# Kernel tuning notes

Hardware: AMD Instinct MI355X
Metric: run time of the kernel (lower is better)

Reference implementation:

```python
import jax, jax.numpy as jnp
import numpy as np

N_NODES = 50000
K_MAX = 10
BATCH = 64
T = 32
N_INPUTS = 16
BITS_PER_FEATURE = 4
INPUT_BITS = N_INPUTS * BITS_PER_FEATURE  # 64


def setup_inputs() -> dict:
    key = jax.random.key(0)
    ks = jax.random.split(key, 8)
    x = jax.random.randint(ks[0], (BATCH, T, INPUT_BITS), 0, 2, dtype=jnp.int32)
    adj_list = jax.random.randint(ks[1], (N_NODES, K_MAX), 0, N_NODES, dtype=jnp.int32)
    adj_list_mask = jax.random.randint(ks[2], (N_NODES, K_MAX), 0, 2, dtype=jnp.int32)
    lut = jax.random.randint(ks[3], (N_NODES, 2 ** K_MAX), 0, 2, dtype=jnp.int32)
    init_states = jax.random.randint(ks[4], (N_NODES,), 0, 2, dtype=jnp.int32)
    input_nodes = jax.random.randint(ks[5], (INPUT_BITS,), 0, N_NODES, dtype=jnp.int32)
    W = jax.random.normal(ks[6], (N_INPUTS, N_NODES), dtype=jnp.float32) * (1.0 / np.sqrt(N_NODES))
    b = jax.random.normal(ks[7], (N_INPUTS,), dtype=jnp.float32) * 0.01
    return {"x": x, "adj_list": adj_list, "adj_list_mask": adj_list_mask,
            "lut": lut, "init_states": init_states, "input_nodes": input_nodes,
            "W": W, "b": b}


def reference(x, adj_list, adj_list_mask, lut, init_states, input_nodes, W, b):
    B, T_, _ = x.shape
    N, K = adj_list.shape
    # powers_of_2 = 2**arange(K).flip()  (MSB-first bit packing)
    pow2 = (2 ** jnp.arange(K - 1, -1, -1)).astype(jnp.int32)  # [K]
    node_ids = jnp.arange(N, dtype=jnp.int32)  # [N]
    s0 = jnp.broadcast_to(init_states[None, :], (B, N)).astype(jnp.int32)

    def step(states, x_t):
        # xor input perturbation at input_nodes
        cur = states[:, input_nodes]                      # [B, INPUT_BITS]
        states = states.at[:, input_nodes].set(jnp.bitwise_xor(cur, x_t))
        # gather masked neighbor states and bit-pack into LUT index
        neigh = jnp.take(states, adj_list, axis=1)        # [B, N, K]
        idx = jnp.sum(neigh * adj_list_mask[None] * pow2, axis=-1)  # [B, N]
        new_states = lut[node_ids[None, :], idx]          # [B, N]
        return new_states, None

    final_states, _ = jax.lax.scan(step, s0, jnp.moveaxis(x, 1, 0))
    # readout = nn.Linear(n_nodes, n_inputs) on final binary states
    out = final_states.astype(jnp.float32) @ W.T + b      # [B, N_INPUTS]
    return out
```

## Files before the change

kernel.cpp:

```cpp
#include <hip/hip_runtime.h>
#include <stdint.h>

#define N_NODES    50000
#define K_MAX      10
#define BATCH      64
#define T_STEPS    32
#define N_INPUTS   16
#define INPUT_BITS 64

#define NPW   256
#define NWG   196
#define NTHR  1024
#define NBUF  (T_STEPS + 1)

#define BUF_STRIDE_B 400128u

#define OFF_BUFS   0u
#define OFF_XMASK  (NBUF * BUF_STRIDE_B)
#define OFF_CTR    (OFF_XMASK + 16384u)
#define OFF_PLUT   (OFF_CTR + 128u)

__global__ void prep_kernel(const int* __restrict__ x,
                            const int* __restrict__ init_states,
                            const int* __restrict__ input_nodes,
                            uint64_t* __restrict__ bufs,
                            uint64_t* __restrict__ xmask,
                            uint32_t* __restrict__ ctr) {
    const int gid = blockIdx.x * blockDim.x + threadIdx.x;
    const size_t strw = BUF_STRIDE_B / 8;
    if (gid < N_NODES) {
        int n = gid;
        int jm = -1;
        for (int j = 0; j < INPUT_BITS; ++j)
            if (input_nodes[j] == n) jm = j;
        uint64_t v = init_states[n] ? ~0ull : 0ull;
        if (jm >= 0) {
            uint64_t m = 0ull;
            for (int b = 0; b < BATCH; ++b)
                m |= (uint64_t)(x[b * (T_STEPS * INPUT_BITS) + jm] & 1) << b;
            v ^= m;
        }
        bufs[n] = v;
    } else if (gid < N_NODES + NBUF) {
        bufs[(size_t)(gid - N_NODES) * strw + N_NODES] = 0ull;
    } else if (gid < N_NODES + NBUF + T_STEPS * INPUT_BITS) {
        int k = gid - (N_NODES + NBUF);
        int t = k >> 6, j = k & 63;
        uint64_t m = 0ull;
        for (int b = 0; b < BATCH; ++b)
            m |= (uint64_t)(x[b * (T_STEPS * INPUT_BITS) + t * INPUT_BITS + j] & 1) << b;
        xmask[k] = m;
    } else if (gid < N_NODES + NBUF + T_STEPS * INPUT_BITS + T_STEPS) {
        ctr[gid - (N_NODES + NBUF + T_STEPS * INPUT_BITS)] = 0;
    }
}

__global__ void lutpack_kernel(const int* __restrict__ lut,
                               uint64_t* __restrict__ plut) {
    const int tid = threadIdx.x;
    const int blk = blockIdx.x;
    const int lane = tid & 63, wave = tid >> 6;
    int v = lut[(size_t)blk * 1024 + tid];
    uint64_t m = __ballot(v & 1);
    if (lane == 0) plut[(size_t)blk * 16 + wave] = m;
}

__global__ __launch_bounds__(NTHR)
void reservoir_coop(const uint64_t* __restrict__ plut,
                    const int* __restrict__ adj,
                    const int* __restrict__ adjmask,
                    const int* __restrict__ input_nodes,
                    const uint64_t* __restrict__ xmask,
                    uint64_t* __restrict__ bufs,
                    uint32_t* __restrict__ ctr) {
    __shared__ uint8_t lutb[NPW * 128];

    const int tid = threadIdx.x;
    const int wg  = blockIdx.x;

    {
        const uint4* src = (const uint4*)(plut + (size_t)wg * NPW * 16);
        uint4* dst = (uint4*)lutb;
        dst[tid * 2]     = src[tid * 2];
        dst[tid * 2 + 1] = src[tid * 2 + 1];
    }

    const int nl   = tid >> 2;
    const int q    = tid & 3;
    const int node = wg * NPW + nl;
    const bool valid = node < N_NODES;
    const uint32_t qsh = (uint32_t)(q & 1) * 16;

    uint32_t off[K_MAX];
    uint32_t soff = 0;
    int jm = -1;
    if (valid) {
        #pragma unroll
        for (int k = 0; k < K_MAX; ++k) {
            int a  = adj[node * K_MAX + k];
            int mk = adjmask[node * K_MAX + k];
            off[k] = (uint32_t)(mk ? a : N_NODES) * 8u + (uint32_t)(q >> 1) * 4u;
        }
        for (int j = 0; j < INPUT_BITS; ++j)
            if (input_nodes[j] == node) jm = j;
        soff = (uint32_t)node * 8u + (uint32_t)(q >> 1) * 4u;
    }
    const int rowbase = nl * 128;
    __syncthreads();

    for (int t = 0; t < T_STEPS; ++t) {
        const char* src = (const char*)bufs + (size_t)t * BUF_STRIDE_B;
        char*       dst = (char*)bufs + (size_t)(t + 1) * BUF_STRIDE_B;
        if (valid) {
            uint32_t w[K_MAX];
            #pragma unroll
            for (int k = 0; k < K_MAX; ++k)
                w[k] = *(const uint32_t*)(src + off[k]) >> qsh;

            uint32_t o16 = 0;
            #pragma unroll
            for (int b = 0; b < 16; ++b) {
                uint32_t idx = 0;
                #pragma unroll
                for (int k = 0; k < K_MAX; ++k)
                    idx = (idx << 1) | ((w[k] >> b) & 1u);
                uint32_t d = *(const uint32_t*)(lutb + rowbase + ((idx >> 5) << 2));
                o16 |= ((d >> (idx & 31)) & 1u) << b;
            }

            uint32_t hi = __shfl_down(o16, 1);
            if ((q & 1) == 0) {
                uint32_t o32 = o16 | (hi << 16);
                if (jm >= 0 && t < T_STEPS - 1)
                    o32 ^= ((const uint32_t*)xmask)[((t + 1) * INPUT_BITS + jm) * 2 + (q >> 1)];
                __hip_atomic_store((uint32_t*)(dst + soff), o32,
                                   __ATOMIC_RELAXED, __HIP_MEMORY_SCOPE_AGENT);
            }
        }

        if (t < T_STEPS - 1) {
            __syncthreads();
            if (tid == 0) {
                __hip_atomic_fetch_add(&ctr[t], 1u, __ATOMIC_RELAXED, __HIP_MEMORY_SCOPE_AGENT);
                while (__hip_atomic_load(&ctr[t], __ATOMIC_RELAXED, __HIP_MEMORY_SCOPE_AGENT)
                       < (uint32_t)NWG)
                    __builtin_amdgcn_s_sleep(2);
            }
            __syncthreads();
        }
    }
}

__global__ void out_kernel(const uint64_t* __restrict__ fstate,
                           const float* __restrict__ W,
                           const float* __restrict__ bias,
                           float* __restrict__ out) {
    const int wg = blockIdx.x;
    const int b = wg >> 4, i = wg & 15;
    const int tid = threadIdx.x;
    const uint8_t* st = (const uint8_t*)fstate;
    const int byteoff = b >> 3, bsh = b & 7;

    float s = 0.f;
    for (int n = tid; n < N_NODES; n += 256) {
        uint32_t bit = (st[(size_t)n * 8 + byteoff] >> bsh) & 1u;
        s += (float)bit * W[(size_t)i * N_NODES + n];
    }
    #pragma unroll
    for (int off = 32; off; off >>= 1) s += __shfl_down(s, off);

    __shared__ float part[4];
    const int lane = tid & 63, wave = tid >> 6;
    if (lane == 0) part[wave] = s;
    __syncthreads();
    if (tid == 0) out[wg] = part[0] + part[1] + part[2] + part[3] + bias[i];
}

extern "C" void kernel_launch(void* const* d_in, const int* in_sizes, int n_in,
                              void* d_out, int out_size, void* d_ws, size_t ws_size,
                              hipStream_t stream) {
    const int*   x       = (const int*)d_in[0];
    const int*   adj     = (const int*)d_in[1];
    const int*   adjmask = (const int*)d_in[2];
    const int*   lut     = (const int*)d_in[3];
    const int*   initst  = (const int*)d_in[4];
    const int*   innodes = (const int*)d_in[5];
    const float* W       = (const float*)d_in[6];
    const float* bias    = (const float*)d_in[7];
    float* out = (float*)d_out;

    char* ws = (char*)d_ws;
    uint64_t* bufs  = (uint64_t*)(ws + OFF_BUFS);
    uint64_t* xmask = (uint64_t*)(ws + OFF_XMASK);
    uint32_t* ctr   = (uint32_t*)(ws + OFF_CTR);
    uint64_t* plut  = (uint64_t*)(ws + OFF_PLUT);

    {
        int prep_threads = N_NODES + NBUF + T_STEPS * INPUT_BITS + T_STEPS;
        int prep_blocks = (prep_threads + 255) / 256;
        hipLaunchKernelGGL(prep_kernel, dim3(prep_blocks), dim3(256), 0, stream,
                           x, initst, innodes, bufs, xmask, ctr);
    }

    hipLaunchKernelGGL(lutpack_kernel, dim3(N_NODES), dim3(1024), 0, stream, lut, plut);

    {
        void* args[] = { (void*)&plut, (void*)&adj, (void*)&adjmask, (void*)&innodes,
                         (void*)&xmask, (void*)&bufs, (void*)&ctr };
        hipLaunchCooperativeKernel((void*)reservoir_coop,
                                   dim3(NWG), dim3(NTHR),
                                   args, 0, stream);
    }

    hipLaunchKernelGGL(out_kernel, dim3(BATCH * N_INPUTS), dim3(256), 0, stream,
                       (const uint64_t*)(ws + OFF_BUFS + (size_t)T_STEPS * BUF_STRIDE_B),
                       W, bias, out);
}
```

Measured before the change: 388.8 us.

## Stage neighbor state words in LDS cooperatively and retune grid to 224 workgroups

Each step, the four threads of a node now split its ten neighbor loads as full 64-bit words, store them in a shared-memory table, and then each thread reads its 16-bit slice from LDS. Before, every thread issued ten scattered 32-bit global loads of its own. The grid goes from 196 workgroups of 1024 threads to 224 workgroups of 896 threads, and each barrier counter gets its own 128-byte slot to avoid false sharing. The cost is an extra __syncthreads per step and some LDS traffic. Any misplacement of the fixed workspace offsets would corrupt data.

```diff
diff --git a/kernel.cpp b/kernel.cpp
--- a/kernel.cpp
+++ b/kernel.cpp
@@ -8,17 +8,17 @@
 #define N_INPUTS   16
 #define INPUT_BITS 64
 
-#define NPW   256
-#define NWG   196
-#define NTHR  1024
+#define NPW   224
+#define NWG   224
+#define NTHR  896
 #define NBUF  (T_STEPS + 1)
 
 #define BUF_STRIDE_B 400128u
 
 #define OFF_BUFS   0u
-#define OFF_XMASK  (NBUF * BUF_STRIDE_B)
-#define OFF_CTR    (OFF_XMASK + 16384u)
-#define OFF_PLUT   (OFF_CTR + 128u)
+#define OFF_XMASK  13204224u
+#define OFF_CTR    13220608u
+#define OFF_PLUT   13224704u
 
 __global__ void prep_kernel(const int* __restrict__ x,
                             const int* __restrict__ init_states,
@@ -50,8 +50,9 @@
         for (int b = 0; b < BATCH; ++b)
             m |= (uint64_t)(x[b * (T_STEPS * INPUT_BITS) + t * INPUT_BITS + j] & 1) << b;
         xmask[k] = m;
-    } else if (gid < N_NODES + NBUF + T_STEPS * INPUT_BITS + T_STEPS) {
-        ctr[gid - (N_NODES + NBUF + T_STEPS * INPUT_BITS)] = 0;
+    } else {
+        int c = gid - (N_NODES + NBUF + T_STEPS * INPUT_BITS);
+        if (c < T_STEPS) ctr[c * 32] = 0;
     }
 }
 
@@ -73,49 +74,62 @@
                     const uint64_t* __restrict__ xmask,
                     uint64_t* __restrict__ bufs,
                     uint32_t* __restrict__ ctr) {
-    __shared__ uint8_t lutb[NPW * 128];
+    __shared__ uint8_t  lutb[NPW * 128];
+    __shared__ uint64_t neigh[NPW * K_MAX];
 
     const int tid = threadIdx.x;
     const int wg  = blockIdx.x;
 
     {
-        const uint4* src = (const uint4*)(plut + (size_t)wg * NPW * 16);
-        uint4* dst = (uint4*)lutb;
-        dst[tid * 2]     = src[tid * 2];
-        dst[tid * 2 + 1] = src[tid * 2 + 1];
+        const uint4* s = (const uint4*)(plut + (size_t)wg * NPW * 16);
+        uint4* d = (uint4*)lutb;
+        d[tid]        = s[tid];
+        d[tid + NTHR] = s[tid + NTHR];
     }
 
     const int nl   = tid >> 2;
     const int q    = tid & 3;
     const int node = wg * NPW + nl;
     const bool valid = node < N_NODES;
-    const uint32_t qsh = (uint32_t)(q & 1) * 16;
-
-    uint32_t off[K_MAX];
-    uint32_t soff = 0;
+
+    uint32_t goff0 = N_NODES, goff1 = N_NODES, goff2 = N_NODES;
     int jm = -1;
     if (valid) {
-        #pragma unroll
-        for (int k = 0; k < K_MAX; ++k) {
-            int a  = adj[node * K_MAX + k];
-            int mk = adjmask[node * K_MAX + k];
-            off[k] = (uint32_t)(mk ? a : N_NODES) * 8u + (uint32_t)(q >> 1) * 4u;
+        int a, mk;
+        a = adj[node * K_MAX + q];      mk = adjmask[node * K_MAX + q];
+        goff0 = mk ? (uint32_t)a : (uint32_t)N_NODES;
+        a = adj[node * K_MAX + q + 4];  mk = adjmask[node * K_MAX + q + 4];
+        goff1 = mk ? (uint32_t)a : (uint32_t)N_NODES;
+        if (q < 2) {
+            a = adj[node * K_MAX + q + 8]; mk = adjmask[node * K_MAX + q + 8];
+            goff2 = mk ? (uint32_t)a : (uint32_t)N_NODES;
         }
         for (int j = 0; j < INPUT_BITS; ++j)
             if (input_nodes[j] == node) jm = j;
-        soff = (uint32_t)node * 8u + (uint32_t)(q >> 1) * 4u;
-    }
-    const int rowbase = nl * 128;
+    }
+    const uint32_t* lut32 = (const uint32_t*)lutb;
+    const uint32_t* xm32  = (const uint32_t*)xmask;
+    const int rowbase = nl * 32;
+    const uint16_t* myrow = (const uint16_t*)neigh + nl * (K_MAX * 4) + q;
     __syncthreads();
 
     for (int t = 0; t < T_STEPS; ++t) {
-        const char* src = (const char*)bufs + (size_t)t * BUF_STRIDE_B;
-        char*       dst = (char*)bufs + (size_t)(t + 1) * BUF_STRIDE_B;
+        const uint64_t* s64 = (const uint64_t*)((const char*)bufs + (size_t)t * BUF_STRIDE_B);
+        uint8_t*        dst = (uint8_t*)bufs + (size_t)(t + 1) * BUF_STRIDE_B;
+
+        uint64_t g0 = s64[goff0];
+        uint64_t g1 = s64[goff1];
+        uint64_t g2 = (q < 2) ? s64[goff2] : 0ull;
+        neigh[nl * K_MAX + q]     = g0;
+        neigh[nl * K_MAX + q + 4] = g1;
+        if (q < 2) neigh[nl * K_MAX + q + 8] = g2;
+        __syncthreads();
+
         if (valid) {
             uint32_t w[K_MAX];
             #pragma unroll
             for (int k = 0; k < K_MAX; ++k)
-                w[k] = *(const uint32_t*)(src + off[k]) >> qsh;
+                w[k] = myrow[k * 4];
 
             uint32_t o16 = 0;
             #pragma unroll
@@ -124,7 +138,7 @@
                 #pragma unroll
                 for (int k = 0; k < K_MAX; ++k)
                     idx = (idx << 1) | ((w[k] >> b) & 1u);
-                uint32_t d = *(const uint32_t*)(lutb + rowbase + ((idx >> 5) << 2));
+                uint32_t d = lut32[rowbase + (idx >> 5)];
                 o16 |= ((d >> (idx & 31)) & 1u) << b;
             }
 
@@ -132,8 +146,8 @@
             if ((q & 1) == 0) {
                 uint32_t o32 = o16 | (hi << 16);
                 if (jm >= 0 && t < T_STEPS - 1)
-                    o32 ^= ((const uint32_t*)xmask)[((t + 1) * INPUT_BITS + jm) * 2 + (q >> 1)];
-                __hip_atomic_store((uint32_t*)(dst + soff), o32,
+                    o32 ^= xm32[((t + 1) * INPUT_BITS + jm) * 2 + (q >> 1)];
+                __hip_atomic_store((uint32_t*)(dst + (size_t)node * 8 + (q & 2) * 2), o32,
                                    __ATOMIC_RELAXED, __HIP_MEMORY_SCOPE_AGENT);
             }
         }
@@ -141,8 +155,9 @@
         if (t < T_STEPS - 1) {
             __syncthreads();
             if (tid == 0) {
-                __hip_atomic_fetch_add(&ctr[t], 1u, __ATOMIC_RELAXED, __HIP_MEMORY_SCOPE_AGENT);
-                while (__hip_atomic_load(&ctr[t], __ATOMIC_RELAXED, __HIP_MEMORY_SCOPE_AGENT)
+                uint32_t* c = ctr + (size_t)t * 32;
+                __hip_atomic_fetch_add(c, 1u, __ATOMIC_RELAXED, __HIP_MEMORY_SCOPE_AGENT);
+                while (__hip_atomic_load(c, __ATOMIC_RELAXED, __HIP_MEMORY_SCOPE_AGENT)
                        < (uint32_t)NWG)
                     __builtin_amdgcn_s_sleep(2);
             }
```

After: 426.5 us. +9.7%, slower.

## Use hierarchical grid barrier and repartition nodes across 224 workgroups

Applied to the files above, without the earlier changes.

Replaces the single global atomic counter barrier with a two-level barrier: workgroups first count into one of 14 group counters, each padded to its own cache line, and the last arrival in each group bumps a root counter that everyone polls. This is meant to cut atomic contention on one address across all workgroups. Nodes are also repartitioned to 224 nodes per workgroup over 224 workgroups of 896 threads, so the grid matches the CU count more closely. The poll sleep is shortened. The cost is an extra atomic hop per barrier and a smaller per-workgroup LUT tile.

```diff
diff --git a/kernel.cpp b/kernel.cpp
--- a/kernel.cpp
+++ b/kernel.cpp
@@ -8,24 +8,28 @@
 #define N_INPUTS   16
 #define INPUT_BITS 64
 
-#define NPW   256
-#define NWG   196
-#define NTHR  1024
+#define NPW   224
+#define NWG   224
+#define NTHR  896
+#define GRPN  14
+#define GRP_SZ 16
 #define NBUF  (T_STEPS + 1)
 
 #define BUF_STRIDE_B 400128u
 
 #define OFF_BUFS   0u
-#define OFF_XMASK  (NBUF * BUF_STRIDE_B)
-#define OFF_CTR    (OFF_XMASK + 16384u)
-#define OFF_PLUT   (OFF_CTR + 128u)
+#define OFF_XMASK  13204224u
+#define OFF_GCTR   13220608u
+#define OFF_RCTR   13335296u
+#define OFF_PLUT   13343488u
 
 __global__ void prep_kernel(const int* __restrict__ x,
                             const int* __restrict__ init_states,
                             const int* __restrict__ input_nodes,
                             uint64_t* __restrict__ bufs,
                             uint64_t* __restrict__ xmask,
-                            uint32_t* __restrict__ ctr) {
+                            uint32_t* __restrict__ gctr,
+                            uint32_t* __restrict__ rctr) {
     const int gid = blockIdx.x * blockDim.x + threadIdx.x;
     const size_t strw = BUF_STRIDE_B / 8;
     if (gid < N_NODES) {
@@ -50,8 +54,11 @@
         for (int b = 0; b < BATCH; ++b)
             m |= (uint64_t)(x[b * (T_STEPS * INPUT_BITS) + t * INPUT_BITS + j] & 1) << b;
         xmask[k] = m;
-    } else if (gid < N_NODES + NBUF + T_STEPS * INPUT_BITS + T_STEPS) {
-        ctr[gid - (N_NODES + NBUF + T_STEPS * INPUT_BITS)] = 0;
+    } else {
+        int c = gid - (N_NODES + NBUF + T_STEPS * INPUT_BITS);
+        if (c < T_STEPS * GRPN) gctr[c * 64] = 0;
+        else if (c < T_STEPS * GRPN + T_STEPS)
+            rctr[(c - T_STEPS * GRPN) * 64] = 0;
     }
 }
 
@@ -72,17 +79,19 @@
                     const int* __restrict__ input_nodes,
                     const uint64_t* __restrict__ xmask,
                     uint64_t* __restrict__ bufs,
-                    uint32_t* __restrict__ ctr) {
+                    uint32_t* __restrict__ gctr,
+                    uint32_t* __restrict__ rctr) {
     __shared__ uint8_t lutb[NPW * 128];
 
     const int tid = threadIdx.x;
     const int wg  = blockIdx.x;
+    const int grp = wg >> 4;
 
     {
-        const uint4* src = (const uint4*)(plut + (size_t)wg * NPW * 16);
-        uint4* dst = (uint4*)lutb;
-        dst[tid * 2]     = src[tid * 2];
-        dst[tid * 2 + 1] = src[tid * 2 + 1];
+        const uint4* s = (const uint4*)(plut + (size_t)wg * NPW * 16);
+        uint4* d = (uint4*)lutb;
+        d[tid]        = s[tid];
+        d[tid + NTHR] = s[tid + NTHR];
     }
 
     const int nl   = tid >> 2;
@@ -105,7 +114,9 @@
             if (input_nodes[j] == node) jm = j;
         soff = (uint32_t)node * 8u + (uint32_t)(q >> 1) * 4u;
     }
-    const int rowbase = nl * 128;
+    const uint32_t* lut32 = (const uint32_t*)lutb;
+    const uint32_t* xm32  = (const uint32_t*)xmask;
+    const int rowbase = nl * 32;
     __syncthreads();
 
     for (int t = 0; t < T_STEPS; ++t) {
@@ -124,7 +135,7 @@
                 #pragma unroll
                 for (int k = 0; k < K_MAX; ++k)
                     idx = (idx << 1) | ((w[k] >> b) & 1u);
-                uint32_t d = *(const uint32_t*)(lutb + rowbase + ((idx >> 5) << 2));
+                uint32_t d = lut32[rowbase + (idx >> 5)];
                 o16 |= ((d >> (idx & 31)) & 1u) << b;
             }
 
@@ -132,7 +143,7 @@
             if ((q & 1) == 0) {
                 uint32_t o32 = o16 | (hi << 16);
                 if (jm >= 0 && t < T_STEPS - 1)
-                    o32 ^= ((const uint32_t*)xmask)[((t + 1) * INPUT_BITS + jm) * 2 + (q >> 1)];
+                    o32 ^= xm32[((t + 1) * INPUT_BITS + jm) * 2 + (q >> 1)];
                 __hip_atomic_store((uint32_t*)(dst + soff), o32,
                                    __ATOMIC_RELAXED, __HIP_MEMORY_SCOPE_AGENT);
             }
@@ -141,10 +152,16 @@
         if (t < T_STEPS - 1) {
             __syncthreads();
             if (tid == 0) {
-                __hip_atomic_fetch_add(&ctr[t], 1u, __ATOMIC_RELAXED, __HIP_MEMORY_SCOPE_AGENT);
-                while (__hip_atomic_load(&ctr[t], __ATOMIC_RELAXED, __HIP_MEMORY_SCOPE_AGENT)
-                       < (uint32_t)NWG)
-                    __builtin_amdgcn_s_sleep(2);
+                uint32_t* gc = gctr + ((size_t)t * GRPN + grp) * 64;
+                uint32_t* rc = rctr + (size_t)t * 64;
+                uint32_t old = __hip_atomic_fetch_add(gc, 1u, __ATOMIC_RELAXED,
+                                                      __HIP_MEMORY_SCOPE_AGENT);
+                if (old == GRP_SZ - 1)
+                    __hip_atomic_fetch_add(rc, 1u, __ATOMIC_RELAXED,
+                                           __HIP_MEMORY_SCOPE_AGENT);
+                while (__hip_atomic_load(rc, __ATOMIC_RELAXED, __HIP_MEMORY_SCOPE_AGENT)
+                       < (uint32_t)GRPN)
+                    __builtin_amdgcn_s_sleep(1);
             }
             __syncthreads();
         }
@@ -192,21 +209,23 @@
     char* ws = (char*)d_ws;
     uint64_t* bufs  = (uint64_t*)(ws + OFF_BUFS);
     uint64_t* xmask = (uint64_t*)(ws + OFF_XMASK);
-    uint32_t* ctr   = (uint32_t*)(ws + OFF_CTR);
+    uint32_t* gctr  = (uint32_t*)(ws + OFF_GCTR);
+    uint32_t* rctr  = (uint32_t*)(ws + OFF_RCTR);
     uint64_t* plut  = (uint64_t*)(ws + OFF_PLUT);
 
     {
-        int prep_threads = N_NODES + NBUF + T_STEPS * INPUT_BITS + T_STEPS;
+        int prep_threads = N_NODES + NBUF + T_STEPS * INPUT_BITS
+                         + T_STEPS * GRPN + T_STEPS;
         int prep_blocks = (prep_threads + 255) / 256;
         hipLaunchKernelGGL(prep_kernel, dim3(prep_blocks), dim3(256), 0, stream,
-                           x, initst, innodes, bufs, xmask, ctr);
+                           x, initst, innodes, bufs, xmask, gctr, rctr);
     }
 
     hipLaunchKernelGGL(lutpack_kernel, dim3(N_NODES), dim3(1024), 0, stream, lut, plut);
 
     {
         void* args[] = { (void*)&plut, (void*)&adj, (void*)&adjmask, (void*)&innodes,
-                         (void*)&xmask, (void*)&bufs, (void*)&ctr };
+                         (void*)&xmask, (void*)&bufs, (void*)&gctr, (void*)&rctr };
         hipLaunchCooperativeKernel((void*)reservoir_coop,
                                    dim3(NWG), dim3(NTHR),
                                    args, 0, stream);
```

Result: faster. 365.0 us (-6.1%).
